# Performance work log

Hardware: AMD Instinct MI355X
Metric: run time of the kernel (lower is better)

The kernel has to match this reference:

```python
import jax, jax.numpy as jnp
import numpy as np

K = 8192
D = 512
BETA = 0.25


def setup_inputs() -> dict:
    key = jax.random.key(0)
    k_z, k_cb = jax.random.split(key)
    z = jax.random.normal(k_z, (8, 4096, D), dtype=jnp.float32)
    codebook = jax.random.normal(k_cb, (K, D), dtype=jnp.float32)
    return {"z": z, "codebook": codebook}


def reference(z, codebook):
    B, Q, Din = z.shape
    flat = z.reshape(-1, Din)                      # (N, D)
    x2 = jnp.sum(flat * flat, axis=1, keepdims=True)   # (N, 1)
    e2 = jnp.sum(codebook * codebook, axis=1)          # (K,)
    xe = flat @ codebook.T                             # (N, K)
    distances = x2 - 2.0 * xe + e2[None, :]
    indices = jnp.argmin(distances, axis=1)            # (N,)
    z_q = codebook[indices].reshape(B, Q, Din)

    codebook_loss = jnp.mean((z_q - jax.lax.stop_gradient(z)) ** 2)
    commitment_loss = jnp.mean((z - jax.lax.stop_gradient(z_q)) ** 2)
    vq_loss = codebook_loss + BETA * commitment_loss
    z_q_ste = z + jax.lax.stop_gradient(z_q - z)

    # perplexity from one-hot usage counts of this batch
    N = flat.shape[0]
    counts = jnp.zeros((codebook.shape[0],), dtype=jnp.float32).at[indices].add(1.0)
    probs = counts / jnp.asarray(N, dtype=jnp.float32)
    perplexity = jnp.exp(-jnp.sum(probs * jnp.log(probs + 1e-10)))

    return z_q_ste, vq_loss, indices.reshape(B, Q), perplexity
```

## Files before the change

kernel.cpp:

```cpp
#include <hip/hip_runtime.h>
#include <hip/hip_bf16.h>

#define K_CODES 8192
#define DIM     512
#define N_VEC   32768
#define MARGIN  0.4f

typedef __attribute__((ext_vector_type(8))) short   short8;
typedef __attribute__((ext_vector_type(8))) unsigned short ushort8;
typedef __attribute__((ext_vector_type(4))) float   float4x;

__device__ inline void gl_lds16(const void* g, void* l) {
    __builtin_amdgcn_global_load_lds(
        (const __attribute__((address_space(1))) unsigned int*)g,
        (__attribute__((address_space(3))) unsigned int*)l, 16, 0, 0);
}

__device__ inline unsigned short f2bf(float f) {
    unsigned int u = __float_as_uint(f);
    return (unsigned short)((u + 0x7FFFu + ((u >> 16) & 1u)) >> 16);
}

__device__ inline float med3(float a, float b, float c) {
    return __builtin_amdgcn_fmed3f(a, b, c);
}

__global__ __launch_bounds__(256) void vq_prep(
    const float* __restrict__ z, const float* __restrict__ cb,
    float* __restrict__ x2, float* __restrict__ hne2,
    unsigned short* __restrict__ zh, unsigned short* __restrict__ ch) {
    int wave = threadIdx.x >> 6;
    int lane = threadIdx.x & 63;
    int row  = blockIdx.x * 4 + wave;
    bool isZ = row < N_VEC;
    int lr = isZ ? row : row - N_VEC;
    const float* src = isZ ? z + (size_t)row * DIM : cb + (size_t)lr * DIM;

    const float4* s4 = (const float4*)src;
    float4 v0 = s4[lane * 2];
    float4 v1 = s4[lane * 2 + 1];
    float f[8] = {v0.x, v0.y, v0.z, v0.w, v1.x, v1.y, v1.z, v1.w};

    float s = 0.0f;
    ushort8 h8;
#pragma unroll
    for (int i = 0; i < 8; ++i) { s += f[i] * f[i]; h8[i] = f2bf(f[i]); }
    ((ushort8*)(isZ ? zh : ch))[(size_t)lr * 64 + lane] = h8;

#pragma unroll
    for (int off = 32; off >= 1; off >>= 1) s += __shfl_xor(s, off, 64);
    if (lane == 0) {
        if (isZ) x2[lr] = s;
        else     hne2[lr] = -0.5f * s;
    }
}

__global__ __launch_bounds__(512, 2) void vq_gemm(
    const unsigned short* __restrict__ zh, const unsigned short* __restrict__ ch,
    const float* __restrict__ hne2,
    float* __restrict__ pP1, float* __restrict__ pP2, float* __restrict__ pP3) {
    __shared__ short8 As[2][2048];
    __shared__ short8 Bs[2][2048];

    const int tid  = threadIdx.x;
    const int w    = tid >> 6;
    const int lane = tid & 63;
    const int wM   = w >> 2;
    const int wN   = w & 3;
    const int rowBase  = blockIdx.x * 256;
    const int codeBase = blockIdx.y * 256;

    const int low3 = lane & 7, m15 = lane & 15, hi4 = lane >> 4;

    unsigned aOff[4], bOff[4];
#pragma unroll
    for (int i = 0; i < 4; ++i) {
        int cell = (w * 4 + i) * 64 + lane;
        int r = cell >> 3, qs = cell & 7, q = qs ^ (r & 7);
        aOff[i] = ((unsigned)(rowBase  + r) * DIM + q * 8) * 2;
        bOff[i] = ((unsigned)(codeBase + r) * DIM + q * 8) * 2;
    }

    int rIdx[8], cIdx[4];
#pragma unroll
    for (int mf = 0; mf < 8; ++mf) rIdx[mf] = (wM * 128 + mf * 16 + m15) * 8;
#pragma unroll
    for (int nf = 0; nf < 4; ++nf) cIdx[nf] = (wN * 64 + nf * 16 + m15) * 8;

    float4x acc[8][4];
#pragma unroll
    for (int mf = 0; mf < 8; ++mf)
#pragma unroll
        for (int nf = 0; nf < 4; ++nf) acc[mf][nf] = (float4x){0.f, 0.f, 0.f, 0.f};

    const char* pA = (const char*)zh;
    const char* pB = (const char*)ch;

#pragma unroll
    for (int i = 0; i < 4; ++i) {
        gl_lds16(pA + aOff[i], &As[0][(w * 4 + i) * 64]);
        gl_lds16(pB + bOff[i], &Bs[0][(w * 4 + i) * 64]);
    }
    __syncthreads();

    int cur = 0;
    for (int t = 0; t < 8; ++t) {
        if (t < 7) {
            const int dc2 = (t + 1) * 128;
#pragma unroll
            for (int i = 0; i < 4; ++i) {
                gl_lds16(pA + aOff[i] + dc2, &As[cur ^ 1][(w * 4 + i) * 64]);
                gl_lds16(pB + bOff[i] + dc2, &Bs[cur ^ 1][(w * 4 + i) * 64]);
            }
        }
#pragma unroll
        for (int ks = 0; ks < 2; ++ks) {
            const int qx = (ks * 4 + hi4) ^ low3;
            short8 a[8];
#pragma unroll
            for (int mf = 0; mf < 8; ++mf) a[mf] = As[cur][rIdx[mf] + qx];
            short8 b[4];
#pragma unroll
            for (int nf = 0; nf < 4; ++nf) b[nf] = Bs[cur][cIdx[nf] + qx];
            __builtin_amdgcn_s_setprio(1);
#pragma unroll
            for (int nf = 0; nf < 4; ++nf)
#pragma unroll
                for (int mf = 0; mf < 8; ++mf)
                    acc[mf][nf] = __builtin_amdgcn_mfma_f32_16x16x32_bf16(
                        a[mf], b[nf], acc[mf][nf], 0, 0, 0);
            __builtin_amdgcn_s_setprio(0);
        }
        __syncthreads();
        cur ^= 1;
    }

    float hv[4];
#pragma unroll
    for (int nf = 0; nf < 4; ++nf)
        hv[nf] = hne2[codeBase + wN * 64 + nf * 16 + m15];

    float G1[8][4], G2[8][4], G3[8][4];
#pragma unroll
    for (int mf = 0; mf < 8; ++mf)
#pragma unroll
        for (int rg = 0; rg < 4; ++rg) {
            G1[mf][rg] = -3.4e38f; G2[mf][rg] = -3.4e38f; G3[mf][rg] = -3.4e38f;
        }

#pragma unroll
    for (int mf = 0; mf < 8; ++mf)
#pragma unroll
        for (int nf = 0; nf < 4; ++nf) {
            unsigned tag = ((unsigned)nf << 4) | (unsigned)m15;
#pragma unroll
            for (int rg = 0; rg < 4; ++rg) {
                float g  = acc[mf][nf][rg] + hv[nf];
                float pk = __uint_as_float(
                    (__float_as_uint(g) & 0xFFFFFFC0u) | tag);
                G3[mf][rg] = med3(pk, G2[mf][rg], G3[mf][rg]);
                G2[mf][rg] = med3(pk, G1[mf][rg], G2[mf][rg]);
                G1[mf][rg] = fmaxf(G1[mf][rg], pk);
            }
        }

    const int slot = blockIdx.y * 4 + wN;
#pragma unroll
    for (int mf = 0; mf < 8; ++mf)
#pragma unroll
        for (int rg = 0; rg < 4; ++rg) {
            float a1 = G1[mf][rg], a2 = G2[mf][rg], a3 = G3[mf][rg];
#pragma unroll
            for (int off = 1; off <= 8; off <<= 1) {
                float b1 = __shfl_xor(a1, off, 64);
                float b2 = __shfl_xor(a2, off, 64);
                float b3 = __shfl_xor(a3, off, 64);
                a3 = med3(b1, a2, a3);
                a2 = med3(b1, a1, a2);
                a1 = fmaxf(a1, b1);
                a3 = med3(b2, a2, a3);
                a2 = med3(b2, a1, a2);
                a3 = med3(b3, a2, a3);
            }
            if (m15 == 0) {
                int row = rowBase + wM * 128 + mf * 16 + hi4 * 4 + rg;
                pP1[(size_t)slot * N_VEC + row] = a1;
                pP2[(size_t)slot * N_VEC + row] = a2;
                pP3[(size_t)slot * N_VEC + row] = a3;
            }
        }
}

__global__ __launch_bounds__(256) void vq_scan(
    const float* __restrict__ pP1, const float* __restrict__ pP2,
    const float* __restrict__ pP3,
    float* __restrict__ pG, int* __restrict__ provIdx, int* __restrict__ flags,
    unsigned long long* __restrict__ keys,
    int* __restrict__ rescueRows, int* __restrict__ rescueCnt,
    int* __restrict__ pairRows, int* __restrict__ pairCnt,
    int* __restrict__ mergedN2) {
    int r = blockIdx.x * 256 + threadIdx.x;
    float g1 = -3.4e38f, g2 = -3.4e38f, g3 = -3.4e38f;
    int   n1 = 0, n2 = 0;
    for (int s = 0; s < 128; ++s) {
        float a1 = pP1[(size_t)s * N_VEC + r];
        float a2 = pP2[(size_t)s * N_VEC + r];
        float a3 = pP3[(size_t)s * N_VEC + r];
        int base = (s >> 2) * 256 + (s & 3) * 64;
        int an1 = base + (int)(__float_as_uint(a1) & 0x3Fu);
        int an2 = base + (int)(__float_as_uint(a2) & 0x3Fu);
        if (a1 > g1)      { g3 = g2; g2 = g1; n2 = n1; g1 = a1; n1 = an1; }
        else if (a1 > g2) { g3 = g2; g2 = a1; n2 = an1; }
        else              g3 = fmaxf(g3, a1);
        if (a2 > g2)      { g3 = g2; g2 = a2; n2 = an2; }
        else              g3 = fmaxf(g3, a2);
        g3 = fmaxf(g3, a3);
    }
    provIdx[r] = n1;
    pG[r] = __uint_as_float(__float_as_uint(g1) & 0xFFFFFFC0u);
    int fl = 0;
    if (g1 - g3 < MARGIN) {
        fl = 1; keys[r] = ~0ull;
        int p = atomicAdd(rescueCnt, 1);
        rescueRows[p] = r;
    } else if (g1 - g2 < MARGIN) {
        fl = 1; keys[r] = ~0ull;
        mergedN2[r] = n2;
        int p = atomicAdd(pairCnt, 1);
        pairRows[p] = r;
    }
    flags[r] = fl;
}

__global__ __launch_bounds__(256) void vq_pair(
    const float* __restrict__ z, const float* __restrict__ cb,
    const float* __restrict__ hne2,
    const int* __restrict__ provIdx, const int* __restrict__ mergedN2,
    const int* __restrict__ pairRows, const int* __restrict__ pairCnt,
    unsigned long long* __restrict__ keys) {
    const int lane = threadIdx.x & 63;
    const int wid  = blockIdx.x * 4 + (threadIdx.x >> 6);
    const int nW   = gridDim.x * 4;
    const int cnt  = *pairCnt;
    for (int i = wid; i < cnt; i += nW) {
        int r  = pairRows[i];
        int n1 = provIdx[r];
        int n2 = mergedN2[r];
        const float4* xz = (const float4*)(z  + (size_t)r  * DIM);
        const float4* c1 = (const float4*)(cb + (size_t)n1 * DIM);
        const float4* c2 = (const float4*)(cb + (size_t)n2 * DIM);
        float4 x0 = xz[lane * 2], x1 = xz[lane * 2 + 1];
        float4 a0 = c1[lane * 2], a1 = c1[lane * 2 + 1];
        float4 b0 = c2[lane * 2], b1 = c2[lane * 2 + 1];
        float d1 = x0.x*a0.x + x0.y*a0.y + x0.z*a0.z + x0.w*a0.w
                 + x1.x*a1.x + x1.y*a1.y + x1.z*a1.z + x1.w*a1.w;
        float d2 = x0.x*b0.x + x0.y*b0.y + x0.z*b0.z + x0.w*b0.w
                 + x1.x*b1.x + x1.y*b1.y + x1.z*b1.z + x1.w*b1.w;
#pragma unroll
        for (int off = 32; off >= 1; off >>= 1) {
            d1 += __shfl_xor(d1, off, 64);
            d2 += __shfl_xor(d2, off, 64);
        }
        if (lane == 0) {
            float kv1 = -hne2[n1] - d1;
            float kv2 = -hne2[n2] - d2;
            int nsel; float kv;
            if (kv2 < kv1 || (kv2 == kv1 && n2 < n1)) { kv = kv2; nsel = n2; }
            else                                      { kv = kv1; nsel = n1; }
            keys[r] = ((unsigned long long)__float_as_uint(kv) << 32) |
                      (unsigned long long)(unsigned)nsel;
        }
    }
}

#define RBM 64
#define RBK 256
#define RBD 32

__global__ __launch_bounds__(256, 2) void vq_rescue(
    const float* __restrict__ z, const float* __restrict__ cb,
    const float* __restrict__ hne2,
    const int* __restrict__ rescueRows, const int* __restrict__ rescueCnt,
    unsigned long long* __restrict__ keys) {
    __shared__ float As[RBD][RBM];
    __shared__ float Bs[RBD][RBK];
    __shared__ int   rowOf[RBM];

    const int tid = threadIdx.x;
    const int tx  = tid & 31;
    const int ty  = tid >> 5;
    const int cnt = *rescueCnt;
    const int codeBase = blockIdx.y * RBK;
    const int sRow = tid >> 2;
    const int sQ   = tid & 3;

    for (int rt = blockIdx.x; rt * RBM < cnt; rt += gridDim.x) {
        const int slotBase = rt * RBM;
        __syncthreads();
        if (tid < RBM) rowOf[tid] = rescueRows[slotBase + tid];
        __syncthreads();

        float acc[8][8];
#pragma unroll
        for (int i = 0; i < 8; ++i)
#pragma unroll
            for (int j = 0; j < 8; ++j) acc[i][j] = 0.0f;

        for (int dc = 0; dc < DIM; dc += RBD) {
            __syncthreads();
            {
                const float* srcA = z + (size_t)rowOf[sRow] * DIM + dc + sQ * 8;
                float4 va0 = ((const float4*)srcA)[0];
                float4 va1 = ((const float4*)srcA)[1];
                int c0 = sQ * 8;
                As[c0 + 0][sRow] = va0.x; As[c0 + 1][sRow] = va0.y;
                As[c0 + 2][sRow] = va0.z; As[c0 + 3][sRow] = va0.w;
                As[c0 + 4][sRow] = va1.x; As[c0 + 5][sRow] = va1.y;
                As[c0 + 6][sRow] = va1.z; As[c0 + 7][sRow] = va1.w;
            }
            {
                const float4* srcB = (const float4*)(cb + (size_t)(codeBase + tid) * DIM + dc);
#pragma unroll
                for (int j = 0; j < 8; ++j) {
                    float4 v = srcB[j];
                    Bs[j * 4 + 0][tid] = v.x; Bs[j * 4 + 1][tid] = v.y;
                    Bs[j * 4 + 2][tid] = v.z; Bs[j * 4 + 3][tid] = v.w;
                }
            }
            __syncthreads();

#pragma unroll
            for (int d = 0; d < RBD; ++d) {
                float a[8], b[8];
                *(float4*)&a[0] = *(const float4*)&As[d][ty * 8];
                *(float4*)&a[4] = *(const float4*)&As[d][ty * 8 + 4];
#pragma unroll
                for (int j = 0; j < 8; ++j) b[j] = Bs[d][tx + 32 * j];
#pragma unroll
                for (int i = 0; i < 8; ++i)
#pragma unroll
                    for (int j = 0; j < 8; ++j) acc[i][j] += a[i] * b[j];
            }
        }

        float best[8];
        int   bidx[8];
#pragma unroll
        for (int i = 0; i < 8; ++i) { best[i] = 3.4e38f; bidx[i] = K_CODES; }

#pragma unroll
        for (int j = 0; j < 8; ++j) {
            int code = codeBase + tx + 32 * j;
            float ev = -hne2[code];
#pragma unroll
            for (int i = 0; i < 8; ++i) {
                float kv = ev - acc[i][j];
                if (kv < best[i] || (kv == best[i] && code < bidx[i])) {
                    best[i] = kv;
                    bidx[i] = code;
                }
            }
        }

#pragma unroll
        for (int off = 16; off >= 1; off >>= 1) {
#pragma unroll
            for (int i = 0; i < 8; ++i) {
                float od = __shfl_xor(best[i], off, 64);
                int   oi = __shfl_xor(bidx[i], off, 64);
                if (od < best[i] || (od == best[i] && oi < bidx[i])) {
                    best[i] = od;
                    bidx[i] = oi;
                }
            }
        }

        if (tx == 0) {
#pragma unroll
            for (int i = 0; i < 8; ++i) {
                int slot = slotBase + ty * 8 + i;
                if (slot < cnt) {
                    unsigned long long key =
                        ((unsigned long long)__float_as_uint(best[i]) << 32) |
                        (unsigned long long)(unsigned)bidx[i];
                    atomicMin(&keys[rowOf[ty * 8 + i]], key);
                }
            }
        }
    }
}

__global__ __launch_bounds__(256) void vq_final(
    const float* __restrict__ gBest, const int* __restrict__ provIdx,
    const int* __restrict__ flags, const unsigned long long* __restrict__ keys,
    const float* __restrict__ x2, const float* __restrict__ cb,
    float* __restrict__ zq, float* __restrict__ idxf,
    float* __restrict__ counts, float* __restrict__ lossAcc) {
    __shared__ int   sIdx[256];
    __shared__ float wsum[4];
    const int tid = threadIdx.x;
    const int r   = blockIdx.x * 256 + tid;

    int n; float dist;
    if (flags[r]) {
        unsigned long long k = keys[r];
        n = (int)(unsigned)(k & 0xffffffffu);
        float kv = __uint_as_float((unsigned)(k >> 32));
        dist = x2[r] + 2.0f * kv;
    } else {
        n = provIdx[r];
        dist = x2[r] - 2.0f * gBest[r];
    }
    sIdx[tid] = n;
    idxf[r]   = (float)n;
    atomicAdd(&counts[n], 1.0f);

    float ls = dist;
#pragma unroll
    for (int off = 32; off >= 1; off >>= 1) ls += __shfl_xor(ls, off, 64);
    if ((tid & 63) == 0) wsum[tid >> 6] = ls;
    __syncthreads();
    if (tid == 0) atomicAdd(lossAcc, wsum[0] + wsum[1] + wsum[2] + wsum[3]);

    const float4* cb4 = (const float4*)cb;
    float4* zq4 = (float4*)(zq + (size_t)blockIdx.x * 256 * DIM);
    for (int t = tid; t < 256 * (DIM / 4); t += 256) {
        int row = t >> 7, f4 = t & 127;
        zq4[(size_t)row * 128 + f4] = cb4[(size_t)sIdx[row] * 128 + f4];
    }
}

__global__ __launch_bounds__(256) void vq_finalize(const float* __restrict__ counts,
                                                   const float* __restrict__ lossAcc,
                                                   float* __restrict__ out_loss,
                                                   float* __restrict__ out_perp) {
    __shared__ float wsum[4];
    int tid = threadIdx.x;
    float s = 0.0f;
    for (int i = tid; i < K_CODES; i += 256) {
        float p = counts[i] * (1.0f / (float)N_VEC);
        s += p * logf(p + 1e-10f);
    }
#pragma unroll
    for (int off = 32; off >= 1; off >>= 1) s += __shfl_xor(s, off, 64);
    if ((tid & 63) == 0) wsum[tid >> 6] = s;
    __syncthreads();
    if (tid == 0) {
        *out_perp = expf(-(wsum[0] + wsum[1] + wsum[2] + wsum[3]));
        *out_loss = 1.25f * lossAcc[0] / (float)(N_VEC * DIM);
    }
}

extern "C" void kernel_launch(void* const* d_in, const int* in_sizes, int n_in,
                              void* d_out, int out_size, void* d_ws, size_t ws_size,
                              hipStream_t stream) {
    (void)in_sizes; (void)n_in; (void)out_size; (void)ws_size;
    const float* z  = (const float*)d_in[0];
    const float* cb = (const float*)d_in[1];

    char* ws = (char*)d_ws;
    float* x2        = (float*)(ws + 0);
    float* hne2      = (float*)(ws + 131072);
    float* counts    = (float*)(ws + 163840);
    float* lossAcc   = (float*)(ws + 196608);
    int*   rescueCnt = (int*)  (ws + 196612);
    int*   pairCnt   = (int*)  (ws + 196616);
    int*   provIdx   = (int*)  (ws + 262144);
    int*   flags     = (int*)  (ws + 393216);
    unsigned long long* keys = (unsigned long long*)(ws + 524288);
    int*   rescueRows = (int*) (ws + 786432);
    float* pG        = (float*)(ws + 1048576);
    int*   mergedN2  = (int*)  (ws + 1179648);
    int*   pairRows  = (int*)  (ws + 1310720);
    unsigned short* zh = (unsigned short*)(ws + 2621440);
    unsigned short* ch = (unsigned short*)(ws + 36175872);

    float* out      = (float*)d_out;
    float* zq       = out;
    float* out_loss = out + 16777216;
    float* idxf     = out + 16777217;
    float* out_perp = out + 16777217 + 32768;

    char* sc = (char*)d_out;
    float* pP1 = (float*)(sc + 0);
    float* pP2 = (float*)(sc + 16777216);
    float* pP3 = (float*)(sc + 33554432);

    hipMemsetAsync(counts, 0, 32768 + 16, stream);
    hipMemsetAsync(rescueRows, 0, 131072, stream);
    vq_prep<<<(N_VEC + K_CODES) / 4, 256, 0, stream>>>(z, cb, x2, hne2, zh, ch);
    dim3 grid(N_VEC / 256, K_CODES / 256);
    vq_gemm<<<grid, 512, 0, stream>>>(zh, ch, hne2, pP1, pP2, pP3);
    vq_scan<<<N_VEC / 256, 256, 0, stream>>>(pP1, pP2, pP3, pG, provIdx, flags,
                                             keys, rescueRows, rescueCnt,
                                             pairRows, pairCnt, mergedN2);
    vq_pair<<<128, 256, 0, stream>>>(z, cb, hne2, provIdx, mergedN2,
                                     pairRows, pairCnt, keys);
    dim3 rgrid(8, 32);
    vq_rescue<<<rgrid, 256, 0, stream>>>(z, cb, hne2, rescueRows, rescueCnt, keys);
    vq_final<<<N_VEC / 256, 256, 0, stream>>>(pG, provIdx, flags, keys, x2, cb,
                                              zq, idxf, counts, lossAcc);
    vq_finalize<<<1, 256, 0, stream>>>(counts, lossAcc, out_loss, out_perp);
}
```

Measured before the change: 722.5 us.

## Deepen GEMM LDS pipeline to four stages and swizzle block order per XCD

The bf16 distance GEMM now splits K into 16 steps of 32 and keeps four LDS buffers in a ring, so three global-to-LDS loads are in flight while one buffer is consumed. Explicit vmcnt waits and raw s_barrier replace the old double buffer with __syncthreads. The grid is flattened to 1D and remapped so that blocks landing on the same XCD (blockIdx mod 8) cover neighbouring code tiles for better L2 reuse. The LDS swizzle is rewritten for the narrower 64-byte rows. The cost is one extra barrier per step and hand-tuned waitcnt values that must exactly match the number of outstanding loads.

Measured after the change: 746.9 us. +3.4%, slower.

```diff
diff --git a/kernel.cpp b/kernel.cpp
--- a/kernel.cpp
+++ b/kernel.cpp
@@ -59,33 +59,40 @@
     const unsigned short* __restrict__ zh, const unsigned short* __restrict__ ch,
     const float* __restrict__ hne2,
     float* __restrict__ pP1, float* __restrict__ pP2, float* __restrict__ pP3) {
-    __shared__ short8 As[2][2048];
-    __shared__ short8 Bs[2][2048];
+    __shared__ short8 As[4][1024];
+    __shared__ short8 Bs[4][1024];
 
     const int tid  = threadIdx.x;
     const int w    = tid >> 6;
     const int lane = tid & 63;
     const int wM   = w >> 2;
     const int wN   = w & 3;
-    const int rowBase  = blockIdx.x * 256;
-    const int codeBase = blockIdx.y * 256;
-
-    const int low3 = lane & 7, m15 = lane & 15, hi4 = lane >> 4;
-
-    unsigned aOff[4], bOff[4];
-#pragma unroll
-    for (int i = 0; i < 4; ++i) {
-        int cell = (w * 4 + i) * 64 + lane;
-        int r = cell >> 3, qs = cell & 7, q = qs ^ (r & 7);
-        aOff[i] = ((unsigned)(rowBase  + r) * DIM + q * 8) * 2;
-        bOff[i] = ((unsigned)(codeBase + r) * DIM + q * 8) * 2;
-    }
-
-    int rIdx[8], cIdx[4];
-#pragma unroll
-    for (int mf = 0; mf < 8; ++mf) rIdx[mf] = (wM * 128 + mf * 16 + m15) * 8;
-#pragma unroll
-    for (int nf = 0; nf < 4; ++nf) cIdx[nf] = (wN * 64 + nf * 16 + m15) * 8;
+
+    const int nsw = (blockIdx.x & 7) * 512 + (blockIdx.x >> 3);
+    const int bx  = nsw >> 5;
+    const int by  = nsw & 31;
+    const int rowBase  = bx * 256;
+    const int codeBase = by * 256;
+
+    const int m15 = lane & 15, hi4 = lane >> 4;
+    const int qsw = hi4 ^ ((m15 >> 1) & 3);
+
+    unsigned aOff[2], bOff[2];
+    int ldsCell[2];
+#pragma unroll
+    for (int i = 0; i < 2; ++i) {
+        int cell = (w * 2 + i) * 64 + lane;
+        int r = cell >> 2, qs = cell & 3, qg = qs ^ ((r >> 1) & 3);
+        aOff[i] = ((unsigned)(rowBase  + r) * DIM + qg * 8) * 2;
+        bOff[i] = ((unsigned)(codeBase + r) * DIM + qg * 8) * 2;
+        ldsCell[i] = (w * 2 + i) * 64;
+    }
+
+    int cA[8], cB[4];
+#pragma unroll
+    for (int mf = 0; mf < 8; ++mf) cA[mf] = (wM * 128 + mf * 16 + m15) * 4 + qsw;
+#pragma unroll
+    for (int nf = 0; nf < 4; ++nf) cB[nf] = (wN * 64 + nf * 16 + m15) * 4 + qsw;
 
     float4x acc[8][4];
 #pragma unroll
@@ -96,44 +103,43 @@
     const char* pA = (const char*)zh;
     const char* pB = (const char*)ch;
 
-#pragma unroll
-    for (int i = 0; i < 4; ++i) {
-        gl_lds16(pA + aOff[i], &As[0][(w * 4 + i) * 64]);
-        gl_lds16(pB + bOff[i], &Bs[0][(w * 4 + i) * 64]);
-    }
-    __syncthreads();
-
-    int cur = 0;
-    for (int t = 0; t < 8; ++t) {
-        if (t < 7) {
-            const int dc2 = (t + 1) * 128;
-#pragma unroll
-            for (int i = 0; i < 4; ++i) {
-                gl_lds16(pA + aOff[i] + dc2, &As[cur ^ 1][(w * 4 + i) * 64]);
-                gl_lds16(pB + bOff[i] + dc2, &Bs[cur ^ 1][(w * 4 + i) * 64]);
-            }
-        }
-#pragma unroll
-        for (int ks = 0; ks < 2; ++ks) {
-            const int qx = (ks * 4 + hi4) ^ low3;
-            short8 a[8];
-#pragma unroll
-            for (int mf = 0; mf < 8; ++mf) a[mf] = As[cur][rIdx[mf] + qx];
-            short8 b[4];
-#pragma unroll
-            for (int nf = 0; nf < 4; ++nf) b[nf] = Bs[cur][cIdx[nf] + qx];
-            __builtin_amdgcn_s_setprio(1);
-#pragma unroll
-            for (int nf = 0; nf < 4; ++nf)
-#pragma unroll
-                for (int mf = 0; mf < 8; ++mf)
-                    acc[mf][nf] = __builtin_amdgcn_mfma_f32_16x16x32_bf16(
-                        a[mf], b[nf], acc[mf][nf], 0, 0, 0);
-            __builtin_amdgcn_s_setprio(0);
-        }
-        __syncthreads();
-        cur ^= 1;
-    }
+#define STAGE(ss, rb)                                             \
+    {                                                             \
+        const unsigned kb = (unsigned)(ss) * 64u;                 \
+        gl_lds16(pA + aOff[0] + kb, &As[rb][ldsCell[0]]);         \
+        gl_lds16(pA + aOff[1] + kb, &As[rb][ldsCell[1]]);         \
+        gl_lds16(pB + bOff[0] + kb, &Bs[rb][ldsCell[0]]);         \
+        gl_lds16(pB + bOff[1] + kb, &Bs[rb][ldsCell[1]]);         \
+    }
+
+    STAGE(0, 0) STAGE(1, 1) STAGE(2, 2)
+
+#pragma unroll
+    for (int s = 0; s < 16; ++s) {
+        if (s < 13) STAGE(s + 3, (s + 3) & 3)
+        if (s < 13)      asm volatile("s_waitcnt vmcnt(12)" ::: "memory");
+        else if (s == 13) asm volatile("s_waitcnt vmcnt(8)" ::: "memory");
+        else if (s == 14) asm volatile("s_waitcnt vmcnt(4)" ::: "memory");
+        else              asm volatile("s_waitcnt vmcnt(0)" ::: "memory");
+        __builtin_amdgcn_s_barrier();
+
+        const int rb = s & 3;
+        short8 a[8], b[4];
+#pragma unroll
+        for (int mf = 0; mf < 8; ++mf) a[mf] = As[rb][cA[mf]];
+#pragma unroll
+        for (int nf = 0; nf < 4; ++nf) b[nf] = Bs[rb][cB[nf]];
+        __builtin_amdgcn_s_setprio(1);
+#pragma unroll
+        for (int nf = 0; nf < 4; ++nf)
+#pragma unroll
+            for (int mf = 0; mf < 8; ++mf)
+                acc[mf][nf] = __builtin_amdgcn_mfma_f32_16x16x32_bf16(
+                    a[mf], b[nf], acc[mf][nf], 0, 0, 0);
+        __builtin_amdgcn_s_setprio(0);
+        __builtin_amdgcn_s_barrier();
+    }
+#undef STAGE
 
     float hv[4];
 #pragma unroll
@@ -164,7 +170,7 @@
             }
         }
 
-    const int slot = blockIdx.y * 4 + wN;
+    const int slot = by * 4 + wN;
 #pragma unroll
     for (int mf = 0; mf < 8; ++mf)
 #pragma unroll
@@ -489,8 +495,7 @@
     hipMemsetAsync(counts, 0, 32768 + 16, stream);
     hipMemsetAsync(rescueRows, 0, 131072, stream);
     vq_prep<<<(N_VEC + K_CODES) / 4, 256, 0, stream>>>(z, cb, x2, hne2, zh, ch);
-    dim3 grid(N_VEC / 256, K_CODES / 256);
-    vq_gemm<<<grid, 512, 0, stream>>>(zh, ch, hne2, pP1, pP2, pP3);
+    vq_gemm<<<4096, 512, 0, stream>>>(zh, ch, hne2, pP1, pP2, pP3);
     vq_scan<<<N_VEC / 256, 256, 0, stream>>>(pP1, pP2, pP3, pG, provIdx, flags,
                                              keys, rescueRows, rescueCnt,
                                              pairRows, pairCnt, mergedN2);
```
